# Performance work log

Hardware: AMD Instinct MI355X
Metric: run time of the kernel (lower is better)

Reference implementation:

```python
import jax, jax.numpy as jnp
import numpy as np

B_CAPS, C_CAPS, KSZ, STRIDE, N_ITER = 32, 32, 3, 2, 3


def setup_inputs() -> dict:
    key = jax.random.key(0)
    k1, k2, k3, k4, k5 = jax.random.split(key, 5)
    b, Bc, Cc, Win = 8, B_CAPS, C_CAPS, 13
    pose = 0.5 * jax.random.normal(k1, (b, 16 * Bc, Win, Win), jnp.float32)
    act = 0.05 + 0.9 * jax.random.uniform(k2, (b, Bc, Win, Win), jnp.float32)
    x = jnp.concatenate([pose, act], axis=1)
    W = 0.3 * jax.random.normal(k3, (KSZ, KSZ, Bc, Cc, 4, 4), jnp.float32)
    beta_v = jax.random.normal(k4, (1,), jnp.float32)
    beta_a = jax.random.normal(k5, (1,), jnp.float32)
    lambda_ = jnp.ones((1,), jnp.float32)
    return {"x": x, "W": W, "beta_v": beta_v, "beta_a": beta_a, "lambda_": lambda_}


def _conv_caps(x, W, beta_v, beta_a, lambda_):
    B, C, K, s, n_iter = B_CAPS, C_CAPS, KSZ, STRIDE, N_ITER
    b, Win = x.shape[0], x.shape[2]
    Wout = (Win - K) // s + 1
    # channel layout of pose is (4,4,B) row-major, per the original .view(-1,4,4,B,...)
    pose = x[:, :-B].reshape(b, 4, 4, B, Win, Win)
    act = x[:, -B:]
    ks = jnp.arange(K)
    Iidx = s * jnp.arange(Wout)[None, :] + ks[:, None]  # (K,Wout): i_in = s*x + ki
    Ir = Iidx[:, None, :, None]  # (K,1,Wout,1)
    Ic = Iidx[None, :, None, :]  # (1,K,1,Wout)
    # pose patches: (b,4,4,B,K,K,Wout,Wout); matrix dims are (q=rows, r=cols)
    pp = pose[:, :, :, :, Ir, Ic]
    # votes[n,o,ki,kj,x,y,c,p,r] = sum_q W[ki,kj,o,c,p,q] * pose[n,q,r,o,ki,kj,x,y]
    votes = jnp.einsum('ijocpq,nqroijxy->noijxycpr', W, pp)
    votes = votes.reshape(b, B, K, K, Wout, Wout, C, 16)
    a_patch = act[:, :, Ir, Ic]  # (b,B,K,K,Wout,Wout)
    # original E-step indexes votes at pos = stride*x - i, which is <=0 and wraps
    # (torch negative indexing) to (-ki) % K.  Faithfully reproduce that permutation.
    kperm = (-ks) % K
    votesE = votes[:, :, kperm][:, :, :, kperm]
    # routing weights kept in patch form R[i_in=s*x+ki, j_in=s*y+kj, x, y] -> (ki,kj,x,y);
    # this is exactly the set of R entries the original ever reads or writes.
    Rp = jnp.full((b, B, K, K, Wout, Wout, C), 1.0 / (Wout * Wout * C), x.dtype)
    TWO_PI = np.float32(2.0 * np.pi)
    lam = jnp.reshape(lambda_, ())
    mu = act_out = None
    for it in range(n_iter):
        # ---- M-step ----
        r_hat = Rp * a_patch[..., None]                      # (b,B,K,K,Wo,Wo,C)
        sum_r = r_hat.sum(axis=(1, 2, 3))                    # (b,Wo,Wo,C)
        mu = jnp.einsum('noijxyc,noijxycd->nxycd', r_hat, votes) / sum_r[..., None]
        mu_b = mu[:, None, None, None]                       # (b,1,1,1,Wo,Wo,C,16)
        sigma = jnp.einsum('noijxyc,noijxycd->nxycd', r_hat, (votes - mu_b) ** 2) / sum_r[..., None]
        cost = (beta_v + jnp.log(sigma)) * sum_r[..., None]  # (b,Wo,Wo,C,16)
        act_out = jax.nn.sigmoid(lam * (beta_a - cost.sum(-1)))  # (b,Wo,Wo,C)
        # ---- E-step (skipped on last iter: its R is never read afterwards) ----
        if it < n_iter - 1:
            # original: p = exp(-(V-mu)^2)/sqrt(2*pi*sigma), prod over 16 pose dims
            p = jnp.prod(jnp.exp(-(votesE - mu_b) ** 2) / jnp.sqrt(TWO_PI * sigma[:, None, None, None]), axis=-1)
            p_hat = act_out[:, None, None, None] * p         # (b,B,K,K,Wo,Wo,C)
            T = p_hat.sum(-1)                                # (b,B,K,K,Wo,Wo)
            # normalizer is per (batch, input-type, input-position): scatter-add over
            # all (ki,x),(kj,y) mapping to the same input pixel, summed over C
            D = jnp.zeros((b, B, Win, Win), x.dtype).at[:, :, Ir, Ic].add(T)
            Rp = p_hat / D[:, :, Ir, Ic][..., None]
    mus = mu.transpose(0, 3, 4, 1, 2).reshape(b, C * 16, Wout, Wout)
    acts = act_out.transpose(0, 3, 1, 2)                     # (b,C,Wo,Wo)
    return jnp.concatenate([mus, acts], axis=1)              # (b, C*17, Wo, Wo)


def reference(x, W, beta_v, beta_a, lambda_):
    return _conv_caps(x, W, beta_v, beta_a, lambda_)
```

## Files before the change

### kernel.cpp

```cpp
#include <hip/hip_runtime.h>


typedef float v2f __attribute__((ext_vector_type(2)));
typedef float v4f __attribute__((ext_vector_type(4)));

#define OFF_PHAT 0
#define OFF_D0   2654208
#define OFF_D1   2697472
#define OFF_POST 2740736
#define OFF_ACTT 3432960
#define OFF_WT2  3476224

__device__ __forceinline__ float wred64(float v) {
#pragma unroll
  for (int m = 32; m >= 1; m >>= 1) v += __shfl_xor(v, m, 64);
  return v;
}

__device__ __forceinline__ v2f lo2(v4f a) { return __builtin_shufflevector(a, a, 0, 1); }
__device__ __forceinline__ v2f hi2(v4f a) { return __builtin_shufflevector(a, a, 2, 3); }

__global__ __launch_bounds__(256) void prep_kernel(
    const float* __restrict__ x, const float* __restrict__ Wt,
    float* __restrict__ posT, float* __restrict__ actT,
    float* __restrict__ Wt2, float* __restrict__ Dz) {
  int tid = blockIdx.x * 256 + threadIdx.x;
  if (tid < 692224) {
    int pix = tid % 169; int t = tid / 169;
    int o = t & 31; t >>= 5;
    int d = t & 15; int n = t >> 4;
    float v = x[((size_t)n * 544 + d * 32 + o) * 169 + pix];
    posT[((size_t)(n * 32 + o) * 169 + pix) * 16 + d] = v;
  } else if (tid < 735488) {
    int r = tid - 692224;
    int pix = r % 169; int t = r / 169;
    int o = t & 31; int n = t >> 5;
    float v = x[(size_t)n * 91936 + 86528 + o * 169 + pix];
    actT[((size_t)n * 169 + pix) * 32 + o] = v;
  } else if (tid < 882944) {
    int r = tid - 735488;
    int c = r / 4608; int s = r - c * 4608;
    int ch = s >> 4, d = s & 15;
    Wt2[r] = Wt[(size_t)ch * 512 + c * 16 + d];
  } else {
    Dz[tid - 882944] = 0.f;
  }
}

__global__ __launch_bounds__(256, 4) void em_kernel(
    const float* __restrict__ Wt2, const float* __restrict__ posT,
    const float* __restrict__ actT, float* __restrict__ p_hat,
    const float* __restrict__ Dread, float* __restrict__ Dwrite,
    const float* __restrict__ beta_v, const float* __restrict__ beta_a,
    const float* __restrict__ lambda_, float* __restrict__ out, int mode) {
  __shared__ float sP[288 * 20];
  __shared__ float sE[288];
  __shared__ float sPh[4 * 288];

  const int g = blockIdx.x & 7;
  const int sg = blockIdx.x >> 3;
  const int wave = threadIdx.x >> 6;
  const int lane = threadIdx.x & 63;
  const int c = g * 4 + wave;

  int t = sg;
  const int y = t % 6; t /= 6;
  const int xx = t % 6;
  const int n = t / 6;

  const float bvv = beta_v[0], bav = beta_a[0], lamv = lambda_[0];
  const float* wbase = Wt2 + (size_t)c * 4608;

  float phv[5];
  if (mode != 0) {
    const float* phb = p_hat + ((size_t)sg * 32 + c) * 288;
#pragma unroll
    for (int k = 0; k < 5; ++k) {
      int ch = lane + 64 * k; if (ch > 287) ch = 287;
      phv[k] = phb[ch];
    }
  }

  for (int task = threadIdx.x; task < 1152; task += 256) {
    int ch = task >> 2, q = task & 3;
    int o = ch & 31, ij = ch >> 5;
    int i = ij / 3, j = ij - i * 3;
    int pix = (2 * xx + i) * 13 + (2 * y + j);
    v4f v = *(const v4f*)(posT +
        ((size_t)((n * 32 + o) * 169) + pix) * 16 + q * 4);
    *(v4f*)(sP + ch * 20 + q * 4) = v;
  }
  for (int task = threadIdx.x; task < 288; task += 256) {
    int o = task & 31, ij = task >> 5;
    int i = ij / 3, j = ij - i * 3;
    int idx = ((size_t)n * 169 + (2 * xx + i) * 13 + (2 * y + j)) * 32 + o;
    float a = actT[idx];
    sE[task] = (mode == 0) ? a * (1.0f / 1152.0f) : a / Dread[idx];
  }
  __syncthreads();

  float sum_r = 0.f;
  v2f sv2[8], sq2[8];
#pragma unroll
  for (int d = 0; d < 8; ++d) { sv2[d] = 0.f; sq2[d] = 0.f; }

#pragma unroll
  for (int k = 0; k < 5; ++k) {
    int ch = lane + 64 * k;
    const bool act_l = (ch < 288);
    const int chm = act_l ? ch : 0;

    const v4f* Pp = (const v4f*)(sP + chm * 20);
    v4f P0 = Pp[0], P1 = Pp[1], P2 = Pp[2], P3 = Pp[3];
    const v4f* Wp = (const v4f*)(wbase + chm * 16);
    v4f W0 = Wp[0], W1 = Wp[1], W2 = Wp[2], W3 = Wp[3];

    float rhat = sE[chm];
    if (mode != 0) rhat *= phv[k];
    if (!act_l) rhat = 0.f;
    sum_r += rhat;

    v2f PL0 = lo2(P0), PH0 = hi2(P0), PL1 = lo2(P1), PH1 = hi2(P1);
    v2f PL2 = lo2(P2), PH2 = hi2(P2), PL3 = lo2(P3), PH3 = hi2(P3);
    v2f r2 = rhat;

#pragma unroll
    for (int p = 0; p < 4; ++p) {
      v4f Wr = (p == 0) ? W0 : (p == 1) ? W1 : (p == 2) ? W2 : W3;
      v2f vlo = Wr.x * PL0 + Wr.y * PL1 + Wr.z * PL2 + Wr.w * PL3;
      v2f vhi = Wr.x * PH0 + Wr.y * PH1 + Wr.z * PH2 + Wr.w * PH3;
      v2f tlo = r2 * vlo, thi = r2 * vhi;
      sv2[p * 2 + 0] += tlo;
      sv2[p * 2 + 1] += thi;
      sq2[p * 2 + 0] += tlo * vlo;
      sq2[p * 2 + 1] += thi * vhi;
    }
  }

  sum_r = wred64(sum_r);
  const float inv_sr = 1.0f / sum_r;
  float mu[16];
  float lsum = 0.f;
#pragma unroll
  for (int d = 0; d < 16; ++d) {
    float s1 = wred64(sv2[d >> 1][d & 1]);
    float s2 = wred64(sq2[d >> 1][d & 1]);
    float m = s1 * inv_sr;
    mu[d] = m;
    float sg_ = fmaxf(s2 * inv_sr - m * m, 1e-30f);
    lsum += __logf(sg_);
  }
  const float cost = (16.f * bvv + lsum) * sum_r;
  const float aout = 1.0f / (1.0f + __expf(-lamv * (bav - cost)));

  if (mode == 2) {
    if (lane == 0) {
      float* ob = out + (size_t)(n * 544 + c * 16) * 36 + xx * 6 + y;
#pragma unroll
      for (int d = 0; d < 16; ++d) ob[d * 36] = mu[d];
      out[(size_t)(n * 544 + 512 + c) * 36 + xx * 6 + y] = aout;
    }
    return;
  }

  v2f mu2[8];
#pragma unroll
  for (int d = 0; d < 8; ++d) { mu2[d].x = mu[2 * d]; mu2[d].y = mu[2 * d + 1]; }
  const float G = __logf(aout) - 0.5f * (lsum + 16.f * 1.8378770664093453f);

#pragma unroll
  for (int k = 0; k < 5; ++k) {
    int mch = lane + 64 * k;
    if (mch < 288) {
      const v4f* Pp = (const v4f*)(sP + mch * 20);
      v4f P0 = Pp[0], P1 = Pp[1], P2 = Pp[2], P3 = Pp[3];
      const v4f* Wp = (const v4f*)(wbase + mch * 16);
      v4f W0 = Wp[0], W1 = Wp[1], W2 = Wp[2], W3 = Wp[3];

      v2f PL0 = lo2(P0), PH0 = hi2(P0), PL1 = lo2(P1), PH1 = hi2(P1);
      v2f PL2 = lo2(P2), PH2 = hi2(P2), PL3 = lo2(P3), PH3 = hi2(P3);
      v2f ss2 = 0.f;
#pragma unroll
      for (int p = 0; p < 4; ++p) {
        v4f Wr = (p == 0) ? W0 : (p == 1) ? W1 : (p == 2) ? W2 : W3;
        v2f vlo = Wr.x * PL0 + Wr.y * PL1 + Wr.z * PL2 + Wr.w * PL3;
        v2f vhi = Wr.x * PH0 + Wr.y * PH1 + Wr.z * PH2 + Wr.w * PH3;
        v2f dlo = vlo - mu2[p * 2 + 0];
        v2f dhi = vhi - mu2[p * 2 + 1];
        ss2 += dlo * dlo;
        ss2 += dhi * dhi;
      }
      float ss = ss2.x + ss2.y;
      float ph = __expf(G - ss);
      int o = mch & 31, ijm = mch >> 5;
      int im = ijm / 3, jm = ijm - im * 3;
      int i2 = (im == 0) ? 0 : 3 - im;
      int j2 = (jm == 0) ? 0 : 3 - jm;
      int slot = (i2 * 3 + j2) * 32 + o;
      p_hat[((size_t)sg * 32 + c) * 288 + slot] = ph;
      sPh[wave * 288 + slot] = ph;
    }
  }
  __syncthreads();
  for (int t2 = threadIdx.x; t2 < 288; t2 += 256) {
    float s = sPh[t2] + sPh[288 + t2] + sPh[576 + t2] + sPh[864 + t2];
    int o = t2 & 31, ij = t2 >> 5;
    int i = ij / 3, j = ij - i * 3;
    atomicAdd(Dwrite + ((size_t)n * 169 + (2 * xx + i) * 13 + (2 * y + j)) * 32 + o, s);
  }
}

extern "C" void kernel_launch(void* const* d_in, const int* in_sizes, int n_in,
                              void* d_out, int out_size, void* d_ws,
                              size_t ws_size, hipStream_t stream) {
  const float* x   = (const float*)d_in[0];
  const float* Wt  = (const float*)d_in[1];
  const float* bv  = (const float*)d_in[2];
  const float* ba  = (const float*)d_in[3];
  const float* lam = (const float*)d_in[4];
  float* out = (float*)d_out;
  float* ws = (float*)d_ws;

  float* p_hat = ws + OFF_PHAT;
  float* D0    = ws + OFF_D0;
  float* D1    = ws + OFF_D1;
  float* posT  = ws + OFF_POST;
  float* actT  = ws + OFF_ACTT;
  float* Wt2   = ws + OFF_WT2;

  (void)in_sizes; (void)n_in; (void)out_size; (void)ws_size;

  prep_kernel<<<3787, 256, 0, stream>>>(x, Wt, posT, actT, Wt2, D0);

  em_kernel<<<2304, 256, 0, stream>>>(Wt2, posT, actT, p_hat, D1, D0,
                                      bv, ba, lam, out, 0);
  em_kernel<<<2304, 256, 0, stream>>>(Wt2, posT, actT, p_hat, D0, D1,
                                      bv, ba, lam, out, 1);
  em_kernel<<<2304, 256, 0, stream>>>(Wt2, posT, actT, p_hat, D1, D0,
                                      bv, ba, lam, out, 2);
}
```

Baseline: 169.0 us.

## Remap EM kernel so each block handles all output capsules of one position

Restructures the EM kernel so one 512-thread block covers all 32 output capsules at a spatial position. Each thread takes one capsule and 18 input channels, where before one wave per capsule walked all 288 channels. This replaces the 64-lane shuffle reductions with a shared-memory cross-group reduction. It also transposes the weights and p_hat so capsule is the fastest dimension for coalesced access, and makes the mode a template parameter. The grid shrinks from 2304 to 288 blocks, which may underfill the GPU and adds extra barriers and per-thread global weight loads.

```diff
diff --git a/kernel.cpp b/kernel.cpp
--- a/kernel.cpp
+++ b/kernel.cpp
@@ -9,21 +9,17 @@
 #define OFF_D1   2697472
 #define OFF_POST 2740736
 #define OFF_ACTT 3432960
-#define OFF_WT2  3476224
-
-__device__ __forceinline__ float wred64(float v) {
-#pragma unroll
-  for (int m = 32; m >= 1; m >>= 1) v += __shfl_xor(v, m, 64);
-  return v;
-}
+#define OFF_WT4  3476224
 
 __device__ __forceinline__ v2f lo2(v4f a) { return __builtin_shufflevector(a, a, 0, 1); }
 __device__ __forceinline__ v2f hi2(v4f a) { return __builtin_shufflevector(a, a, 2, 3); }
+
+__device__ __constant__ int kp_c[9] = {0, 2, 1, 6, 8, 7, 3, 5, 4};
 
 __global__ __launch_bounds__(256) void prep_kernel(
     const float* __restrict__ x, const float* __restrict__ Wt,
     float* __restrict__ posT, float* __restrict__ actT,
-    float* __restrict__ Wt2, float* __restrict__ Dz) {
+    float* __restrict__ Wt4, float* __restrict__ Dz) {
   int tid = blockIdx.x * 256 + threadIdx.x;
   if (tid < 692224) {
     int pix = tid % 169; int t = tid / 169;
@@ -39,29 +35,34 @@
     actT[((size_t)n * 169 + pix) * 32 + o] = v;
   } else if (tid < 882944) {
     int r = tid - 735488;
-    int c = r / 4608; int s = r - c * 4608;
-    int ch = s >> 4, d = s & 15;
-    Wt2[r] = Wt[(size_t)ch * 512 + c * 16 + d];
+    int c = r & 31;
+    int d = (r >> 5) & 15;
+    int ch = r >> 9;
+    Wt4[r] = Wt[(size_t)ch * 512 + c * 16 + d];
   } else {
     Dz[tid - 882944] = 0.f;
   }
 }
 
-__global__ __launch_bounds__(256, 4) void em_kernel(
-    const float* __restrict__ Wt2, const float* __restrict__ posT,
+template <int MODE>
+__global__ __launch_bounds__(512) void em_kernel(
+    const float* __restrict__ Wt4, const float* __restrict__ posT,
     const float* __restrict__ actT, float* __restrict__ p_hat,
     const float* __restrict__ Dread, float* __restrict__ Dwrite,
     const float* __restrict__ beta_v, const float* __restrict__ beta_a,
-    const float* __restrict__ lambda_, float* __restrict__ out, int mode) {
-  __shared__ float sP[288 * 20];
+    const float* __restrict__ lambda_, float* __restrict__ out) {
+  __shared__ float sP[288 * 16];
   __shared__ float sE[288];
-  __shared__ float sPh[4 * 288];
-
-  const int g = blockIdx.x & 7;
-  const int sg = blockIdx.x >> 3;
-  const int wave = threadIdx.x >> 6;
-  const int lane = threadIdx.x & 63;
-  const int c = g * 4 + wave;
+  __shared__ float sRed[8 * 32 * 37];
+  __shared__ float sMu[32 * 20];
+  __shared__ float sL[32 * 17];
+  __shared__ float sG[32];
+
+  const int tid = threadIdx.x;
+  const int c = tid & 31;
+  const int grp = tid >> 5;
+  const int wv = tid >> 6;
+  const int sg = blockIdx.x;
 
   int t = sg;
   const int y = t % 6; t /= 6;
@@ -69,33 +70,22 @@
   const int n = t / 6;
 
   const float bvv = beta_v[0], bav = beta_a[0], lamv = lambda_[0];
-  const float* wbase = Wt2 + (size_t)c * 4608;
-
-  float phv[5];
-  if (mode != 0) {
-    const float* phb = p_hat + ((size_t)sg * 32 + c) * 288;
-#pragma unroll
-    for (int k = 0; k < 5; ++k) {
-      int ch = lane + 64 * k; if (ch > 287) ch = 287;
-      phv[k] = phb[ch];
-    }
-  }
-
-  for (int task = threadIdx.x; task < 1152; task += 256) {
+
+  for (int task = tid; task < 1152; task += 512) {
     int ch = task >> 2, q = task & 3;
     int o = ch & 31, ij = ch >> 5;
     int i = ij / 3, j = ij - i * 3;
     int pix = (2 * xx + i) * 13 + (2 * y + j);
     v4f v = *(const v4f*)(posT +
         ((size_t)((n * 32 + o) * 169) + pix) * 16 + q * 4);
-    *(v4f*)(sP + ch * 20 + q * 4) = v;
-  }
-  for (int task = threadIdx.x; task < 288; task += 256) {
+    *(v4f*)(sP + ch * 16 + q * 4) = v;
+  }
+  for (int task = tid; task < 288; task += 512) {
     int o = task & 31, ij = task >> 5;
     int i = ij / 3, j = ij - i * 3;
     int idx = ((size_t)n * 169 + (2 * xx + i) * 13 + (2 * y + j)) * 32 + o;
     float a = actT[idx];
-    sE[task] = (mode == 0) ? a * (1.0f / 1152.0f) : a / Dread[idx];
+    sE[task] = (MODE == 0) ? a * (1.0f / 1152.0f) : a / Dread[idx];
   }
   __syncthreads();
 
@@ -104,107 +94,117 @@
 #pragma unroll
   for (int d = 0; d < 8; ++d) { sv2[d] = 0.f; sq2[d] = 0.f; }
 
-#pragma unroll
-  for (int k = 0; k < 5; ++k) {
-    int ch = lane + 64 * k;
-    const bool act_l = (ch < 288);
-    const int chm = act_l ? ch : 0;
-
-    const v4f* Pp = (const v4f*)(sP + chm * 20);
-    v4f P0 = Pp[0], P1 = Pp[1], P2 = Pp[2], P3 = Pp[3];
-    const v4f* Wp = (const v4f*)(wbase + chm * 16);
-    v4f W0 = Wp[0], W1 = Wp[1], W2 = Wp[2], W3 = Wp[3];
-
-    float rhat = sE[chm];
-    if (mode != 0) rhat *= phv[k];
-    if (!act_l) rhat = 0.f;
+  const int ch0 = grp * 18;
+#pragma unroll 2
+  for (int ch = ch0; ch < ch0 + 18; ++ch) {
+    const float* wp = Wt4 + (size_t)ch * 512 + c;
+    float w[16];
+#pragma unroll
+    for (int d = 0; d < 16; ++d) w[d] = wp[d * 32];
+    const v4f* Pp = (const v4f*)(sP + ch * 16);
+    v4f Pq0 = Pp[0], Pq1 = Pp[1], Pq2 = Pp[2], Pq3 = Pp[3];
+
+    float rhat = sE[ch];
+    if (MODE != 0) rhat *= p_hat[((size_t)sg * 288 + ch) * 32 + c];
     sum_r += rhat;
 
-    v2f PL0 = lo2(P0), PH0 = hi2(P0), PL1 = lo2(P1), PH1 = hi2(P1);
-    v2f PL2 = lo2(P2), PH2 = hi2(P2), PL3 = lo2(P3), PH3 = hi2(P3);
-    v2f r2 = rhat;
-
 #pragma unroll
     for (int p = 0; p < 4; ++p) {
-      v4f Wr = (p == 0) ? W0 : (p == 1) ? W1 : (p == 2) ? W2 : W3;
-      v2f vlo = Wr.x * PL0 + Wr.y * PL1 + Wr.z * PL2 + Wr.w * PL3;
-      v2f vhi = Wr.x * PH0 + Wr.y * PH1 + Wr.z * PH2 + Wr.w * PH3;
-      v2f tlo = r2 * vlo, thi = r2 * vhi;
-      sv2[p * 2 + 0] += tlo;
-      sv2[p * 2 + 1] += thi;
-      sq2[p * 2 + 0] += tlo * vlo;
-      sq2[p * 2 + 1] += thi * vhi;
-    }
-  }
-
-  sum_r = wred64(sum_r);
-  const float inv_sr = 1.0f / sum_r;
-  float mu[16];
-  float lsum = 0.f;
-#pragma unroll
-  for (int d = 0; d < 16; ++d) {
-    float s1 = wred64(sv2[d >> 1][d & 1]);
-    float s2 = wred64(sq2[d >> 1][d & 1]);
-    float m = s1 * inv_sr;
-    mu[d] = m;
-    float sg_ = fmaxf(s2 * inv_sr - m * m, 1e-30f);
-    lsum += __logf(sg_);
-  }
-  const float cost = (16.f * bvv + lsum) * sum_r;
-  const float aout = 1.0f / (1.0f + __expf(-lamv * (bav - cost)));
-
-  if (mode == 2) {
-    if (lane == 0) {
-      float* ob = out + (size_t)(n * 544 + c * 16) * 36 + xx * 6 + y;
-#pragma unroll
-      for (int d = 0; d < 16; ++d) ob[d * 36] = mu[d];
+      v4f vote = w[p * 4 + 0] * Pq0 + w[p * 4 + 1] * Pq1 +
+                 w[p * 4 + 2] * Pq2 + w[p * 4 + 3] * Pq3;
+      v2f vl = lo2(vote), vh = hi2(vote);
+      v2f tl = rhat * vl, th = rhat * vh;
+      sv2[2 * p] += tl;     sv2[2 * p + 1] += th;
+      sq2[2 * p] += tl * vl; sq2[2 * p + 1] += th * vh;
+    }
+  }
+
+  sum_r += __shfl_xor(sum_r, 32);
+#pragma unroll
+  for (int i = 0; i < 8; ++i) {
+    sv2[i].x += __shfl_xor(sv2[i].x, 32);
+    sv2[i].y += __shfl_xor(sv2[i].y, 32);
+    sq2[i].x += __shfl_xor(sq2[i].x, 32);
+    sq2[i].y += __shfl_xor(sq2[i].y, 32);
+  }
+  if ((tid & 63) < 32) {
+    float* r = sRed + (wv * 32 + c) * 37;
+    r[0] = sum_r;
+#pragma unroll
+    for (int d = 0; d < 16; ++d) {
+      r[1 + d] = sv2[d >> 1][d & 1];
+      r[17 + d] = sq2[d >> 1][d & 1];
+    }
+  }
+  __syncthreads();
+
+  const int d = grp;
+  float S = 0.f, svd = 0.f, sqd = 0.f;
+#pragma unroll
+  for (int g = 0; g < 8; ++g) {
+    const float* r = sRed + (g * 32 + c) * 37;
+    S += r[0]; svd += r[1 + d]; sqd += r[17 + d];
+  }
+  const float inv_sr = 1.0f / S;
+  const float m = svd * inv_sr;
+  const float sg_ = fmaxf(sqd * inv_sr - m * m, 1e-30f);
+  sMu[c * 20 + d] = m;
+  sL[c * 17 + d] = __logf(sg_);
+  __syncthreads();
+
+  if (grp == 0) {
+    float ls = 0.f;
+#pragma unroll
+    for (int dd = 0; dd < 16; ++dd) ls += sL[c * 17 + dd];
+    const float cost = (16.f * bvv + ls) * S;
+    const float aout = 1.0f / (1.0f + __expf(-lamv * (bav - cost)));
+    if (MODE == 2) {
       out[(size_t)(n * 544 + 512 + c) * 36 + xx * 6 + y] = aout;
-    }
+    } else {
+      sG[c] = __logf(aout) - 0.5f * (ls + 16.f * 1.8378770664093453f);
+    }
+  }
+  if (MODE == 2) {
+    out[(size_t)(n * 544 + c * 16 + d) * 36 + xx * 6 + y] = m;
     return;
   }
-
-  v2f mu2[8];
-#pragma unroll
-  for (int d = 0; d < 8; ++d) { mu2[d].x = mu[2 * d]; mu2[d].y = mu[2 * d + 1]; }
-  const float G = __logf(aout) - 0.5f * (lsum + 16.f * 1.8378770664093453f);
-
-#pragma unroll
-  for (int k = 0; k < 5; ++k) {
-    int mch = lane + 64 * k;
-    if (mch < 288) {
-      const v4f* Pp = (const v4f*)(sP + mch * 20);
-      v4f P0 = Pp[0], P1 = Pp[1], P2 = Pp[2], P3 = Pp[3];
-      const v4f* Wp = (const v4f*)(wbase + mch * 16);
-      v4f W0 = Wp[0], W1 = Wp[1], W2 = Wp[2], W3 = Wp[3];
-
-      v2f PL0 = lo2(P0), PH0 = hi2(P0), PL1 = lo2(P1), PH1 = hi2(P1);
-      v2f PL2 = lo2(P2), PH2 = hi2(P2), PL3 = lo2(P3), PH3 = hi2(P3);
-      v2f ss2 = 0.f;
-#pragma unroll
-      for (int p = 0; p < 4; ++p) {
-        v4f Wr = (p == 0) ? W0 : (p == 1) ? W1 : (p == 2) ? W2 : W3;
-        v2f vlo = Wr.x * PL0 + Wr.y * PL1 + Wr.z * PL2 + Wr.w * PL3;
-        v2f vhi = Wr.x * PH0 + Wr.y * PH1 + Wr.z * PH2 + Wr.w * PH3;
-        v2f dlo = vlo - mu2[p * 2 + 0];
-        v2f dhi = vhi - mu2[p * 2 + 1];
-        ss2 += dlo * dlo;
-        ss2 += dhi * dhi;
-      }
-      float ss = ss2.x + ss2.y;
-      float ph = __expf(G - ss);
-      int o = mch & 31, ijm = mch >> 5;
-      int im = ijm / 3, jm = ijm - im * 3;
-      int i2 = (im == 0) ? 0 : 3 - im;
-      int j2 = (jm == 0) ? 0 : 3 - jm;
-      int slot = (i2 * 3 + j2) * 32 + o;
-      p_hat[((size_t)sg * 32 + c) * 288 + slot] = ph;
-      sPh[wave * 288 + slot] = ph;
-    }
-  }
-  __syncthreads();
-  for (int t2 = threadIdx.x; t2 < 288; t2 += 256) {
-    float s = sPh[t2] + sPh[288 + t2] + sPh[576 + t2] + sPh[864 + t2];
-    int o = t2 & 31, ij = t2 >> 5;
+  __syncthreads();
+  const float G = sG[c];
+  const v4f* mup = (const v4f*)(sMu + c * 20);
+  v4f mu0 = mup[0], mu1 = mup[1], mu2v = mup[2], mu3 = mup[3];
+
+#pragma unroll 2
+  for (int ch = ch0; ch < ch0 + 18; ++ch) {
+    const float* wp = Wt4 + (size_t)ch * 512 + c;
+    float w[16];
+#pragma unroll
+    for (int dd = 0; dd < 16; ++dd) w[dd] = wp[dd * 32];
+    const v4f* Pp = (const v4f*)(sP + ch * 16);
+    v4f Pq0 = Pp[0], Pq1 = Pp[1], Pq2 = Pp[2], Pq3 = Pp[3];
+
+    v4f ssa = 0.f;
+#pragma unroll
+    for (int p = 0; p < 4; ++p) {
+      v4f vote = w[p * 4 + 0] * Pq0 + w[p * 4 + 1] * Pq1 +
+                 w[p * 4 + 2] * Pq2 + w[p * 4 + 3] * Pq3;
+      v4f mu_p = (p == 0) ? mu0 : (p == 1) ? mu1 : (p == 2) ? mu2v : mu3;
+      v4f dif = vote - mu_p;
+      ssa += dif * dif;
+    }
+    float ss = ssa.x + ssa.y + ssa.z + ssa.w;
+    float ph = __expf(G - ss);
+    int slot = kp_c[ch >> 5] * 32 + (ch & 31);
+    p_hat[((size_t)sg * 288 + slot) * 32 + c] = ph;
+  }
+  __syncthreads();
+
+  if (tid < 288) {
+    const float* pb = p_hat + ((size_t)sg * 288 + tid) * 32;
+    v4f a0 = 0.f;
+#pragma unroll
+    for (int q = 0; q < 8; ++q) a0 += ((const v4f*)pb)[q];
+    float s = a0.x + a0.y + a0.z + a0.w;
+    int o = tid & 31, ij = tid >> 5;
     int i = ij / 3, j = ij - i * 3;
     atomicAdd(Dwrite + ((size_t)n * 169 + (2 * xx + i) * 13 + (2 * y + j)) * 32 + o, s);
   }
@@ -226,16 +226,16 @@
   float* D1    = ws + OFF_D1;
   float* posT  = ws + OFF_POST;
   float* actT  = ws + OFF_ACTT;
-  float* Wt2   = ws + OFF_WT2;
+  float* Wt4   = ws + OFF_WT4;
 
   (void)in_sizes; (void)n_in; (void)out_size; (void)ws_size;
 
-  prep_kernel<<<3787, 256, 0, stream>>>(x, Wt, posT, actT, Wt2, D0);
-
-  em_kernel<<<2304, 256, 0, stream>>>(Wt2, posT, actT, p_hat, D1, D0,
-                                      bv, ba, lam, out, 0);
-  em_kernel<<<2304, 256, 0, stream>>>(Wt2, posT, actT, p_hat, D0, D1,
-                                      bv, ba, lam, out, 1);
-  em_kernel<<<2304, 256, 0, stream>>>(Wt2, posT, actT, p_hat, D1, D0,
-                                      bv, ba, lam, out, 2);
+  prep_kernel<<<3787, 256, 0, stream>>>(x, Wt, posT, actT, Wt4, D0);
+
+  em_kernel<0><<<288, 512, 0, stream>>>(Wt4, posT, actT, p_hat, D1, D0,
+                                        bv, ba, lam, out);
+  em_kernel<1><<<288, 512, 0, stream>>>(Wt4, posT, actT, p_hat, D0, D1,
+                                        bv, ba, lam, out);
+  em_kernel<2><<<288, 512, 0, stream>>>(Wt4, posT, actT, p_hat, D1, D0,
+                                        bv, ba, lam, out);
 }
```

Result: slower. 181.1 us (+7.1%).
